# Performance work log

Hardware: AMD Instinct MI355X
Metric: run time of the kernel (lower is better)

## Reference

```python
import jax, jax.numpy as jnp
import numpy as np

N_BASE = 4          # len('NACGT'[1:])
STATE_LEN = 5
S = N_BASE ** STATE_LEN   # 1024 states
NZ = N_BASE + 1           # 5 transitions per state
T_STEPS = 800
BATCH = 32


def _build_idx():
    # idx[i] = [i, 0*256 + i//4, 1*256 + i//4, 2*256 + i//4, 3*256 + i//4]
    i = np.arange(S)
    trans = np.stack([j * (S // N_BASE) + i // N_BASE for j in range(N_BASE)], axis=1)
    idx = np.concatenate([i[:, None], trans], axis=1).astype(np.int64)      # (S, NZ)
    # transposed transition structure (stable sort: duplicates grouped deterministically)
    idx_T = np.argsort(idx.ravel(), kind='stable').reshape(S, NZ)
    idx_T_div = idx_T // NZ
    return jnp.asarray(idx), jnp.asarray(idx_T), jnp.asarray(idx_T_div)


def _scan(Ms, idx, v0):
    """Log-semiring recurrence: alpha[t+1] = logsumexp(Ms[t] + alpha[t][:, idx], -1).
    Ms: (T, N, S, NZ); idx: (S, NZ); v0: (N, S). Returns (T+1, N, S)."""
    def step(alpha, M):
        nxt = jax.scipy.special.logsumexp(M + alpha[:, idx], axis=-1)  # (N, S)
        return nxt, nxt
    _, alphas = jax.lax.scan(step, v0, Ms)
    return jnp.concatenate([v0[None], alphas], axis=0)


def setup_inputs() -> dict:
    key = jax.random.key(0)
    scores = jax.random.normal(key, (T_STEPS, BATCH, S * NZ), dtype=jnp.float32)
    return {"scores": scores}


def reference(scores):
    idx, idx_T, idx_T_div = _build_idx()
    T, N, _ = scores.shape
    Ms = scores.reshape(T, N, S, NZ)
    v0 = jnp.zeros((N, S), scores.dtype)   # semiring Log.one == 0.0
    # forward scores
    fwd = _scan(Ms, idx, v0)                                   # (T+1, N, S)
    # backward scores: gather transposed transitions, run scan in reverse time
    Ms_T = scores[:, :, idx_T]                                 # (T, N, S, NZ)
    bwd = jnp.flip(_scan(jnp.flip(Ms_T, 0), idx_T_div, v0), 0)  # (T+1, N, S)
    posts = jax.nn.softmax(fwd + bwd, axis=-1)                 # (T+1, N, S)
    return (jnp.swapaxes(scores, 0, 1),
            jnp.swapaxes(bwd, 0, 1),
            jnp.swapaxes(posts, 0, 1))
```

## Files before the change

### kernel.cpp

```cpp
#include <hip/hip_runtime.h>
#include <stdint.h>

#define T_STEPS 800
#define NBATCH  32
#define SST     1024
#define ROW     5120
#define RING    5

#define SCAN_BLOCKS 64

__device__ __forceinline__ float lse5(float v0, float v1, float v2, float v3, float v4) {
  float m = fmaxf(fmaxf(fmaxf(v0, v1), fmaxf(v2, v3)), v4);
  float s = __expf(v0 - m) + __expf(v1 - m) + __expf(v2 - m) +
            __expf(v3 - m) + __expf(v4 - m);
  return m + __logf(s);
}

#define WAITVM(N) do { \
  asm volatile("s_waitcnt vmcnt(" #N ")" ::: "memory"); \
  __builtin_amdgcn_sched_barrier(0); } while (0)

__device__ __forceinline__ void barrier_lgkm() {
  asm volatile("s_waitcnt lgkmcnt(0)" ::: "memory");
  __builtin_amdgcn_s_barrier();
  asm volatile("" ::: "memory");
}

__device__ __forceinline__ void stage16(const float* g, float* l) {
  __builtin_amdgcn_global_load_lds(
      (const __attribute__((address_space(1))) uint32_t*)g,
      (__attribute__((address_space(3))) uint32_t*)l, 16, 0, 0);
}

__device__ __forceinline__ void stage_row(const float* __restrict__ rowg,
                                          float* __restrict__ ldsrow,
                                          int w, int lane) {
  const float* src = rowg + 1280 * w + 4 * lane;
  float* dst = ldsrow + 1280 * w;
#pragma unroll
  for (int k = 0; k < 5; ++k) stage16(src + 256 * k, dst + 256 * k);
}

template <int DIR, int PHASE>
__device__ __forceinline__ void step_one(int s, int buf, int u, int w, int lane,
                                         float* __restrict__ outn,
                                         float* __restrict__ o0n,
                                         const float* __restrict__ base,
                                         float (*ring)[ROW], float (*abuf)[SST],
                                         float (&a)[4]) {
  if constexpr (PHASE == 0)      WAITVM(21);
  else if constexpr (PHASE == 1) { if constexpr (DIR) WAITVM(44); else WAITVM(36); }
  else                           WAITVM(0);

  if constexpr (DIR) barrier_lgkm();

  const int cur = s & 1;
  const int nxt = cur ^ 1;
  const int t = DIR ? (T_STEPS - 1 - s) : s;
  const float* rb = ring[buf];

  float4 q[5];
  const float4* rv = (const float4*)(rb + 20 * u);
#pragma unroll
  for (int m = 0; m < 5; ++m) q[m] = rv[m];
  float fv[20];
#pragma unroll
  for (int m = 0; m < 5; ++m) {
    fv[4 * m + 0] = q[m].x; fv[4 * m + 1] = q[m].y;
    fv[4 * m + 2] = q[m].z; fv[4 * m + 3] = q[m].w;
  }
  float sv[4];
  if constexpr (DIR) {
#pragma unroll
    for (int j = 0; j < 4; ++j) sv[j] = rb[5 * u + 1280 * j];
  }

  float4 pv;
  if constexpr (!DIR) {
    pv.x = abuf[cur][u];
    pv.y = abuf[cur][u + 256];
    pv.z = abuf[cur][u + 512];
    pv.w = abuf[cur][u + 768];
  } else {
    pv = *(const float4*)&abuf[cur][4 * u];
  }

  float na[4];
#pragma unroll
  for (int j = 0; j < 4; ++j) {
    float w0, w1, w2, w3, w4;
    if constexpr (!DIR) {
      w0 = fv[5 * j + 0] + a[j];
      w1 = fv[5 * j + 1] + pv.x;
      w2 = fv[5 * j + 2] + pv.y;
      w3 = fv[5 * j + 3] + pv.z;
      w4 = fv[5 * j + 4] + pv.w;
    } else {
      w0 = sv[j]          + a[j];
      w1 = fv[1 + j + 0]  + pv.x;
      w2 = fv[1 + j + 5]  + pv.y;
      w3 = fv[1 + j + 10] + pv.z;
      w4 = fv[1 + j + 15] + pv.w;
    }
    na[j] = lse5(w0, w1, w2, w3, w4);
    a[j] = na[j];
  }

  {
    float* o0 = o0n + (size_t)t * ROW + 1280 * w + 4 * lane;
    const float* qb = rb + 1280 * w + 4 * lane;
    if constexpr (!DIR) {
#pragma unroll
      for (int c = 0; c < 5; c += 2)
        *(float4*)(o0 + 256 * c) = *(const float4*)(qb + 256 * c);
    } else {
#pragma unroll
      for (int c = 1; c < 5; c += 2)
        *(float4*)(o0 + 256 * c) = *(const float4*)(qb + 256 * c);
    }
  }

  if constexpr (!DIR) {
    const float4 o = {na[0], na[1], na[2], na[3]};
    ((float4*)(outn + (size_t)(s + 1) * SST))[u] = o;
    *(float4*)&abuf[nxt][4 * u] = o;
  } else {
#pragma unroll
    for (int j = 0; j < 4; ++j) {
      outn[(size_t)t * SST + u + 256 * j] = na[j];
      abuf[nxt][u + 256 * j] = na[j];
    }
  }

  barrier_lgkm();

  if constexpr (PHASE != 2) {
    const int tn = DIR ? (T_STEPS - 1 - (s + RING)) : (s + RING);
    stage_row(base + (size_t)tn * (NBATCH * ROW), ring[buf], w, lane);
  }
}

template <int DIR>
__device__ void scan_run(const float* __restrict__ scores, float* __restrict__ out,
                         float* __restrict__ out0, int n,
                         float (*ring)[ROW], float (*abuf)[SST]) {
  const int u = threadIdx.x;
  const int w = u >> 6, lane = u & 63;
  const float* base = scores + (size_t)n * ROW;
  float* outn = out + (size_t)n * (T_STEPS + 1) * SST;
  float* o0n  = out0 + (size_t)n * T_STEPS * ROW;
  float a[4] = {0.f, 0.f, 0.f, 0.f};

#pragma unroll
  for (int i = 0; i < RING; ++i) {
    const int t = DIR ? (T_STEPS - 1 - i) : i;
    stage_row(base + (size_t)t * (NBATCH * ROW), ring[i], w, lane);
  }
  {
    const float4 z = {0.f, 0.f, 0.f, 0.f};
    *(float4*)&abuf[0][4 * u] = z;
    const size_t t0 = DIR ? (size_t)T_STEPS : 0;
    ((float4*)(outn + t0 * SST))[u] = z;
  }
  barrier_lgkm();

#pragma unroll
  for (int i = 0; i < RING; ++i)
    step_one<DIR, 0>(i, i, u, w, lane, outn, o0n, base, ring, abuf, a);

  for (int p = RING; p < T_STEPS - RING; p += RING) {
#pragma unroll
    for (int i = 0; i < RING; ++i)
      step_one<DIR, 1>(p + i, i, u, w, lane, outn, o0n, base, ring, abuf, a);
  }

#pragma unroll
  for (int i = 0; i < RING; ++i)
    step_one<DIR, 2>(T_STEPS - RING + i, i, u, w, lane, outn, o0n, base, ring, abuf, a);
}

__global__ __launch_bounds__(256) void mega(const float* __restrict__ scores,
                                            float* __restrict__ out0,
                                            float* __restrict__ bwdo,
                                            float* __restrict__ fposts) {
  __shared__ float ring[RING][ROW];
  __shared__ float abuf[2][SST];
  const int b = blockIdx.x;
  if (b < NBATCH) scan_run<0>(scores, fposts, out0, b, ring, abuf);
  else            scan_run<1>(scores, bwdo,   out0, b - NBATCH, ring, abuf);
}

__global__ __launch_bounds__(256) void posts_kernel(float* __restrict__ fp,
                                                    const float* __restrict__ bp) {
  const int lane = threadIdx.x & 63;
  const int wid  = threadIdx.x >> 6;
  const size_t row = (size_t)blockIdx.x * 4 + wid;
  float* f = fp + row * SST;
  const float* b = bp + row * SST;

  float x[16];
#pragma unroll
  for (int k = 0; k < 4; ++k) {
    const float4 fv = ((const float4*)f)[lane + 64 * k];
    const float4 bv = ((const float4*)b)[lane + 64 * k];
    x[4 * k + 0] = fv.x + bv.x;
    x[4 * k + 1] = fv.y + bv.y;
    x[4 * k + 2] = fv.z + bv.z;
    x[4 * k + 3] = fv.w + bv.w;
  }
  float m = x[0];
#pragma unroll
  for (int j = 1; j < 16; ++j) m = fmaxf(m, x[j]);
#pragma unroll
  for (int off = 32; off >= 1; off >>= 1) m = fmaxf(m, __shfl_xor(m, off));
  float ssum = 0.0f;
#pragma unroll
  for (int j = 0; j < 16; ++j) { x[j] = __expf(x[j] - m); ssum += x[j]; }
#pragma unroll
  for (int off = 32; off >= 1; off >>= 1) ssum += __shfl_xor(ssum, off);
  const float inv = 1.0f / ssum;
#pragma unroll
  for (int k = 0; k < 4; ++k) {
    float4 o;
    o.x = x[4 * k + 0] * inv;
    o.y = x[4 * k + 1] * inv;
    o.z = x[4 * k + 2] * inv;
    o.w = x[4 * k + 3] * inv;
    ((float4*)f)[lane + 64 * k] = o;
  }
}

extern "C" void kernel_launch(void* const* d_in, const int* in_sizes, int n_in,
                              void* d_out, int out_size, void* d_ws, size_t ws_size,
                              hipStream_t stream) {
  (void)in_sizes; (void)n_in; (void)d_ws; (void)ws_size; (void)out_size;
  const float* scores = (const float*)d_in[0];
  float* out = (float*)d_out;
  float* out0   = out;
  float* bwdo   = out + (size_t)NBATCH * T_STEPS * ROW;
  float* fposts = bwdo + (size_t)NBATCH * (T_STEPS + 1) * SST;

  mega<<<SCAN_BLOCKS, 256, 0, stream>>>(scores, out0, bwdo, fposts);
  posts_kernel<<<(NBATCH * (T_STEPS + 1)) / 4, 256, 0, stream>>>(fposts, bwdo);
}
```

Measured before the change: 703.5 us.

## Software-pipeline LDS row reads one step ahead of the scan recurrence

Moves the per-step LDS loads of score rows (and the out0 copy-through stores) into a prefetch that runs right after the current step's alpha update, so the next step's operands are already in registers. The ring slot is now a template parameter, the vmcnt wait thresholds are retuned, and a single barrier per step replaces the separate pre and post barriers for the backward direction. The goal is to take LDS latency and the copy traffic off the serial critical path of the recurrence. In exchange it adds register pressure from carrying fv/sv across steps, relies on hand-counted vmcnt values, and forces a single block per CU via launch bounds.

```diff
diff --git a/kernel.cpp b/kernel.cpp
--- a/kernel.cpp
+++ b/kernel.cpp
@@ -41,39 +41,50 @@
   for (int k = 0; k < 5; ++k) stage16(src + 256 * k, dst + 256 * k);
 }
 
-template <int DIR, int PHASE>
-__device__ __forceinline__ void step_one(int s, int buf, int u, int w, int lane,
+template <int DIR>
+__device__ __forceinline__ void prefetch_row(const float* __restrict__ rb,
+                                             float* __restrict__ o0n, int trow,
+                                             int u, int w, int lane,
+                                             float (&fv)[20], float (&sv)[4]) {
+  const float4* rv = (const float4*)(rb + 20 * u);
+#pragma unroll
+  for (int m = 0; m < 5; ++m) {
+    const float4 q = rv[m];
+    fv[4 * m + 0] = q.x; fv[4 * m + 1] = q.y;
+    fv[4 * m + 2] = q.z; fv[4 * m + 3] = q.w;
+  }
+  if constexpr (DIR) {
+#pragma unroll
+    for (int j = 0; j < 4; ++j) sv[j] = rb[5 * u + 1280 * j];
+  }
+  float* o0 = o0n + (size_t)trow * ROW + 1280 * w + 4 * lane;
+  const float* qb = rb + 1280 * w + 4 * lane;
+  if constexpr (!DIR) {
+#pragma unroll
+    for (int c = 0; c < 5; c += 2)
+      *(float4*)(o0 + 256 * c) = *(const float4*)(qb + 256 * c);
+  } else {
+#pragma unroll
+    for (int c = 1; c < 5; c += 2)
+      *(float4*)(o0 + 256 * c) = *(const float4*)(qb + 256 * c);
+  }
+}
+
+template <int DIR, int PHASE, int SLOT>
+__device__ __forceinline__ void step_one(int s, int u, int w, int lane,
                                          float* __restrict__ outn,
                                          float* __restrict__ o0n,
                                          const float* __restrict__ base,
                                          float (*ring)[ROW], float (*abuf)[SST],
+                                         float (&fv)[20], float (&sv)[4],
                                          float (&a)[4]) {
-  if constexpr (PHASE == 0)      WAITVM(21);
-  else if constexpr (PHASE == 1) { if constexpr (DIR) WAITVM(44); else WAITVM(36); }
-  else                           WAITVM(0);
-
-  if constexpr (DIR) barrier_lgkm();
+  if constexpr (PHASE == 0)      { if constexpr (DIR) WAITVM(18); else WAITVM(19); }
+  else if constexpr (PHASE == 1) { if constexpr (DIR) WAITVM(33); else WAITVM(27); }
+  else                           { WAITVM(0); }
+  barrier_lgkm();
 
   const int cur = s & 1;
   const int nxt = cur ^ 1;
-  const int t = DIR ? (T_STEPS - 1 - s) : s;
-  const float* rb = ring[buf];
-
-  float4 q[5];
-  const float4* rv = (const float4*)(rb + 20 * u);
-#pragma unroll
-  for (int m = 0; m < 5; ++m) q[m] = rv[m];
-  float fv[20];
-#pragma unroll
-  for (int m = 0; m < 5; ++m) {
-    fv[4 * m + 0] = q[m].x; fv[4 * m + 1] = q[m].y;
-    fv[4 * m + 2] = q[m].z; fv[4 * m + 3] = q[m].w;
-  }
-  float sv[4];
-  if constexpr (DIR) {
-#pragma unroll
-    for (int j = 0; j < 4; ++j) sv[j] = rb[5 * u + 1280 * j];
-  }
 
   float4 pv;
   if constexpr (!DIR) {
@@ -106,25 +117,12 @@
     a[j] = na[j];
   }
 
-  {
-    float* o0 = o0n + (size_t)t * ROW + 1280 * w + 4 * lane;
-    const float* qb = rb + 1280 * w + 4 * lane;
-    if constexpr (!DIR) {
-#pragma unroll
-      for (int c = 0; c < 5; c += 2)
-        *(float4*)(o0 + 256 * c) = *(const float4*)(qb + 256 * c);
-    } else {
-#pragma unroll
-      for (int c = 1; c < 5; c += 2)
-        *(float4*)(o0 + 256 * c) = *(const float4*)(qb + 256 * c);
-    }
-  }
-
   if constexpr (!DIR) {
     const float4 o = {na[0], na[1], na[2], na[3]};
     ((float4*)(outn + (size_t)(s + 1) * SST))[u] = o;
     *(float4*)&abuf[nxt][4 * u] = o;
   } else {
+    const int t = T_STEPS - 1 - s;
 #pragma unroll
     for (int j = 0; j < 4; ++j) {
       outn[(size_t)t * SST + u + 256 * j] = na[j];
@@ -132,12 +130,17 @@
     }
   }
 
-  barrier_lgkm();
-
+  if (s + 1 < T_STEPS) {
+    const int trow = DIR ? (T_STEPS - 2 - s) : (s + 1);
+    prefetch_row<DIR>(ring[(SLOT + 1) % RING], o0n, trow, u, w, lane, fv, sv);
+  }
+
+  __builtin_amdgcn_sched_barrier(0);
   if constexpr (PHASE != 2) {
-    const int tn = DIR ? (T_STEPS - 1 - (s + RING)) : (s + RING);
-    stage_row(base + (size_t)tn * (NBATCH * ROW), ring[buf], w, lane);
-  }
+    const int trow = DIR ? (T_STEPS - 1 - (s + RING)) : (s + RING);
+    stage_row(base + (size_t)trow * (NBATCH * ROW), ring[SLOT], w, lane);
+  }
+  __builtin_amdgcn_sched_barrier(0);
 }
 
 template <int DIR>
@@ -149,6 +152,7 @@
   const float* base = scores + (size_t)n * ROW;
   float* outn = out + (size_t)n * (T_STEPS + 1) * SST;
   float* o0n  = out0 + (size_t)n * T_STEPS * ROW;
+  float fv[20], sv[4];
   float a[4] = {0.f, 0.f, 0.f, 0.f};
 
 #pragma unroll
@@ -162,27 +166,35 @@
     const size_t t0 = DIR ? (size_t)T_STEPS : 0;
     ((float4*)(outn + t0 * SST))[u] = z;
   }
+  WAITVM(21);
   barrier_lgkm();
-
-#pragma unroll
-  for (int i = 0; i < RING; ++i)
-    step_one<DIR, 0>(i, i, u, w, lane, outn, o0n, base, ring, abuf, a);
+  prefetch_row<DIR>(ring[0], o0n, DIR ? (T_STEPS - 1) : 0, u, w, lane, fv, sv);
+
+  step_one<DIR, 0, 0>(0, u, w, lane, outn, o0n, base, ring, abuf, fv, sv, a);
+  step_one<DIR, 0, 1>(1, u, w, lane, outn, o0n, base, ring, abuf, fv, sv, a);
+  step_one<DIR, 0, 2>(2, u, w, lane, outn, o0n, base, ring, abuf, fv, sv, a);
+  step_one<DIR, 0, 3>(3, u, w, lane, outn, o0n, base, ring, abuf, fv, sv, a);
+  step_one<DIR, 1, 4>(4, u, w, lane, outn, o0n, base, ring, abuf, fv, sv, a);
 
   for (int p = RING; p < T_STEPS - RING; p += RING) {
-#pragma unroll
-    for (int i = 0; i < RING; ++i)
-      step_one<DIR, 1>(p + i, i, u, w, lane, outn, o0n, base, ring, abuf, a);
-  }
-
-#pragma unroll
-  for (int i = 0; i < RING; ++i)
-    step_one<DIR, 2>(T_STEPS - RING + i, i, u, w, lane, outn, o0n, base, ring, abuf, a);
-}
-
-__global__ __launch_bounds__(256) void mega(const float* __restrict__ scores,
-                                            float* __restrict__ out0,
-                                            float* __restrict__ bwdo,
-                                            float* __restrict__ fposts) {
+    step_one<DIR, 1, 0>(p + 0, u, w, lane, outn, o0n, base, ring, abuf, fv, sv, a);
+    step_one<DIR, 1, 1>(p + 1, u, w, lane, outn, o0n, base, ring, abuf, fv, sv, a);
+    step_one<DIR, 1, 2>(p + 2, u, w, lane, outn, o0n, base, ring, abuf, fv, sv, a);
+    step_one<DIR, 1, 3>(p + 3, u, w, lane, outn, o0n, base, ring, abuf, fv, sv, a);
+    step_one<DIR, 1, 4>(p + 4, u, w, lane, outn, o0n, base, ring, abuf, fv, sv, a);
+  }
+
+  step_one<DIR, 2, 0>(795, u, w, lane, outn, o0n, base, ring, abuf, fv, sv, a);
+  step_one<DIR, 2, 1>(796, u, w, lane, outn, o0n, base, ring, abuf, fv, sv, a);
+  step_one<DIR, 2, 2>(797, u, w, lane, outn, o0n, base, ring, abuf, fv, sv, a);
+  step_one<DIR, 2, 3>(798, u, w, lane, outn, o0n, base, ring, abuf, fv, sv, a);
+  step_one<DIR, 2, 4>(799, u, w, lane, outn, o0n, base, ring, abuf, fv, sv, a);
+}
+
+__global__ __launch_bounds__(256, 1) void mega(const float* __restrict__ scores,
+                                               float* __restrict__ out0,
+                                               float* __restrict__ bwdo,
+                                               float* __restrict__ fposts) {
   __shared__ float ring[RING][ROW];
   __shared__ float abuf[2][SST];
   const int b = blockIdx.x;
```

After: 698.9 us. Within noise of the previous version (-0.7%).
